# Optimization experiments

Measured on AMD Instinct MI355X. Metric: run time of the kernel, lower is better.

The kernel has to match this reference:

```python
import jax, jax.numpy as jnp
import numpy as np

N_NODES = 100000
N_EDGES = 1000000
N_GRAPHS = 512
HID = 64
EDIM = 32
LAYERS = 4
BN_EPS = 1e-5


def _batchnorm(x, g, b):
    # training-mode BatchNorm1d: biased batch statistics over the node axis
    m = x.mean(axis=0)
    v = jnp.var(x, axis=0)
    return (x - m) * jax.lax.rsqrt(v + BN_EPS) * g + b


def setup_inputs() -> dict:
    key = jax.random.key(0)
    ks = jax.random.split(key, 16)
    zw = 2 * HID + EDIM  # 160: cat([x_i, x_j, e_ij])
    inp = {
        "z": jax.random.randint(ks[0], (N_NODES,), 0, 100),
        "edge_index": jax.random.randint(ks[1], (2, N_EDGES), 0, N_NODES),
        "edge_attr": jax.random.normal(ks[2], (N_EDGES, EDIM), dtype=jnp.float32),
        "batch_ids": jnp.sort(jax.random.randint(ks[3], (N_NODES,), 0, N_GRAPHS)),
        "emb": jax.random.normal(ks[4], (100, HID), dtype=jnp.float32),
        "Wf": jax.random.normal(ks[5], (LAYERS, zw, HID), dtype=jnp.float32) / np.sqrt(zw),
        "bf": jnp.zeros((LAYERS, HID), jnp.float32),
        "Ws": jax.random.normal(ks[6], (LAYERS, zw, HID), dtype=jnp.float32) / np.sqrt(zw),
        "bs": jnp.zeros((LAYERS, HID), jnp.float32),
        "g_cbn": jnp.ones((LAYERS, HID), jnp.float32),
        "b_cbn": jnp.zeros((LAYERS, HID), jnp.float32),
        "g_obn": jnp.ones((LAYERS, HID), jnp.float32),
        "b_obn": jnp.zeros((LAYERS, HID), jnp.float32),
        "W1": jax.random.normal(ks[7], (HID, HID), dtype=jnp.float32) / np.sqrt(HID),
        "b1": jnp.zeros((HID,), jnp.float32),
        "W2": jax.random.normal(ks[8], (HID, 1), dtype=jnp.float32) / np.sqrt(HID),
        "b2": jnp.zeros((1,), jnp.float32),
    }
    return inp


def reference(z, edge_index, edge_attr, batch_ids, emb, Wf, bf, Ws, bs,
              g_cbn, b_cbn, g_obn, b_obn, W1, b1, W2, b2):
    src = edge_index[0]  # x_j (source)
    dst = edge_index[1]  # x_i (target / aggregation index)
    x = emb[z]  # [N, HID]
    for l in range(LAYERS):
        # CGConv message: z_e = cat([x_i, x_j, e_ij]); m = sigmoid(f(z_e)) * softplus(s(z_e))
        z_e = jnp.concatenate([x[dst], x[src], edge_attr], axis=-1)  # [E, 160]
        msg = jax.nn.sigmoid(z_e @ Wf[l] + bf[l]) * jax.nn.softplus(z_e @ Ws[l] + bs[l])
        agg = jax.ops.segment_sum(msg, dst, num_segments=N_NODES)  # [N, HID]
        agg = _batchnorm(agg, g_cbn[l], b_cbn[l])  # CGConv's internal BN
        x = agg + x  # residual
        x = _batchnorm(x, g_obn[l], b_obn[l])  # outer BatchNorm1d
        x = jax.nn.softplus(x)
    # global mean pool over graphs
    sums = jax.ops.segment_sum(x, batch_ids, num_segments=N_GRAPHS)
    cnts = jax.ops.segment_sum(jnp.ones((N_NODES,), x.dtype), batch_ids, num_segments=N_GRAPHS)
    pooled = sums / jnp.maximum(cnts, 1.0)[:, None]
    h = jax.nn.silu(pooled @ W1 + b1)  # dropout is identity in eval mode
    out = (h @ W2 + b2)[:, 0]
    return out
```

## Files before the change

### kernel.cpp

```cpp
#include <hip/hip_runtime.h>
#include <cstdint>
#include <cstddef>

#define N_NODES 100000
#define N_EDGES 1000000
#define N_GRAPHS 512
#define HID 64
#define EDIM 32
#define LAYERS 4
#define BN_EPS 1e-5
#define NPB 1024

static const size_t X_OFF    = 0;
static const size_t AGG_OFF  = 25600000;
static const size_t STA_OFF  = 51200000;
static const size_t STB_OFF  = 51201024;
static const size_t POOL_OFF = 51202048;
static const size_t CNT_OFF  = 51333120;
static const size_t DEG_OFF  = 51335168;
static const size_t ECUR_OFF = 51735296;
static const size_t PERM_OFF = 52135424;
static const size_t DSTS_OFF = 56135424;
static const size_t SRCS_OFF = 60135424;
static const size_t BSUM_OFF = 64135424;
static const size_t BOFF_OFF = 64137472;
static const size_t PART_OFF = 64139520;
static const size_t P_OFF    = 64663808;

#define SCAN_BLOCKS 391

__device__ __forceinline__ float rl_f(float v, int k) {
    return __uint_as_float(__builtin_amdgcn_readlane(__float_as_uint(v), k));
}
__device__ __forceinline__ float sigmoidf_(float x) {
    return 1.f / (1.f + __expf(-x));
}
__device__ __forceinline__ float softplusf_(float x) {
    return fmaxf(x, 0.f) + __logf(1.f + __expf(-fabsf(x)));
}
__device__ __forceinline__ void fma4(float4& a, const float4& wv, float xv) {
    a.x = fmaf(xv, wv.x, a.x);
    a.y = fmaf(xv, wv.y, a.y);
    a.z = fmaf(xv, wv.z, a.z);
    a.w = fmaf(xv, wv.w, a.w);
}

__global__ __launch_bounds__(256) void cg_embed(const int* __restrict__ z,
                                                const float* __restrict__ emb,
                                                float* __restrict__ x) {
    int i = blockIdx.x * 256 + threadIdx.x;
    if (i < N_NODES * HID) {
        x[i] = emb[z[i >> 6] * HID + (i & 63)];
    }
}

__global__ __launch_bounds__(256) void cg_hist(const int* __restrict__ ei,
                                               int* __restrict__ deg) {
    int e = blockIdx.x * 256 + threadIdx.x;
    if (e < N_EDGES) atomicAdd(&deg[ei[N_EDGES + e]], 1);
}

__global__ __launch_bounds__(256) void cg_bsum(const int* __restrict__ deg,
                                               int* __restrict__ bsum) {
    const int i = blockIdx.x * 256 + threadIdx.x;
    int v = (i < N_NODES) ? deg[i] : 0;
#pragma unroll
    for (int off = 32; off > 0; off >>= 1) v += __shfl_down(v, off);
    __shared__ int wsum[4];
    if ((threadIdx.x & 63) == 0) wsum[threadIdx.x >> 6] = v;
    __syncthreads();
    if (threadIdx.x == 0) bsum[blockIdx.x] = wsum[0] + wsum[1] + wsum[2] + wsum[3];
}

__global__ __launch_bounds__(512) void cg_bscan(const int* __restrict__ bsum,
                                                int* __restrict__ boff) {
    __shared__ int ps[512];
    const int t = threadIdx.x;
    int v = (t < SCAN_BLOCKS) ? bsum[t] : 0;
    ps[t] = v;
    __syncthreads();
    for (int off = 1; off < 512; off <<= 1) {
        int u = (t >= off) ? ps[t - off] : 0;
        __syncthreads();
        ps[t] += u;
        __syncthreads();
    }
    if (t < SCAN_BLOCKS) boff[t] = ps[t] - v;
}

__global__ __launch_bounds__(256) void cg_escan(const int* __restrict__ deg,
                                                const int* __restrict__ boff,
                                                int* __restrict__ ecur) {
    __shared__ int ps[256];
    const int t = threadIdx.x;
    const int i = blockIdx.x * 256 + t;
    int v = (i < N_NODES) ? deg[i] : 0;
    ps[t] = v;
    __syncthreads();
    for (int off = 1; off < 256; off <<= 1) {
        int u = (t >= off) ? ps[t - off] : 0;
        __syncthreads();
        ps[t] += u;
        __syncthreads();
    }
    if (i < N_NODES) ecur[i] = ps[t] - v + boff[blockIdx.x];
}

__global__ __launch_bounds__(256) void cg_scatter(const int* __restrict__ ei,
                                                  int* __restrict__ ecur,
                                                  int* __restrict__ perm,
                                                  int* __restrict__ dst_s,
                                                  int* __restrict__ src_s) {
    int e = blockIdx.x * 256 + threadIdx.x;
    if (e < N_EDGES) {
        int d = ei[N_EDGES + e];
        int pos = atomicAdd(&ecur[d], 1);
        perm[pos] = e;
        dst_s[pos] = d;
        src_s[pos] = ei[e];
    }
}

__global__ __launch_bounds__(256, 2) void cg_nodeP4(const float* __restrict__ x,
                                                    const float* __restrict__ Wf,
                                                    const float* __restrict__ Ws,
                                                    float* __restrict__ P) {
    __shared__ __align__(16) float xs[64][68];
    const int tid = threadIdx.x;
    const int base = blockIdx.x * 64;
#pragma unroll
    for (int i = 0; i < 4; i++) {
        int f4 = tid * 4 + i;
        int r = f4 >> 4, c4 = (f4 & 15) * 4;
        float4 v = {0, 0, 0, 0};
        if (base + r < N_NODES) v = *(const float4*)(x + (size_t)(base + r) * HID + c4);
        *(float4*)(&xs[r][c4]) = v;
    }
    __syncthreads();

    const int g = tid >> 4;
    const int j4 = (tid & 15) * 4;
    float4 acc[4][4];
#pragma unroll
    for (int m = 0; m < 4; m++)
#pragma unroll
        for (int q = 0; q < 4; q++) acc[m][q] = {0, 0, 0, 0};

    for (int k = 0; k < 64; k++) {
        float4 w0 = *(const float4*)(Wf + (size_t)k * HID + j4);
        float4 w1 = *(const float4*)(Ws + (size_t)k * HID + j4);
        float4 w2 = *(const float4*)(Wf + (size_t)(64 + k) * HID + j4);
        float4 w3 = *(const float4*)(Ws + (size_t)(64 + k) * HID + j4);
#pragma unroll
        for (int m = 0; m < 4; m++) {
            float xv = xs[g + m * 16][k];
            fma4(acc[m][0], w0, xv);
            fma4(acc[m][1], w1, xv);
            fma4(acc[m][2], w2, xv);
            fma4(acc[m][3], w3, xv);
        }
    }
#pragma unroll
    for (int m = 0; m < 4; m++) {
        int r = base + g + m * 16;
        if (r < N_NODES) {
            float* o = P + (size_t)r * 256;
            *(float4*)(o + j4)       = acc[m][0];
            *(float4*)(o + 64 + j4)  = acc[m][1];
            *(float4*)(o + 128 + j4) = acc[m][2];
            *(float4*)(o + 192 + j4) = acc[m][3];
        }
    }
}

__global__ __launch_bounds__(256, 4) void cg_edge4(const float* __restrict__ P,
                                                   const float* __restrict__ ea,
                                                   const int* __restrict__ perm,
                                                   const int* __restrict__ dst_s,
                                                   const int* __restrict__ src_s,
                                                   const float* __restrict__ WfE,
                                                   const float* __restrict__ WsE,
                                                   const float* __restrict__ bf,
                                                   const float* __restrict__ bs,
                                                   float* __restrict__ agg) {
    const int j = threadIdx.x & 63;
    float wfe[EDIM], wse[EDIM];
#pragma unroll
    for (int k = 0; k < EDIM; k++) wfe[k] = WfE[k * HID + j];
#pragma unroll
    for (int k = 0; k < EDIM; k++) wse[k] = WsE[k * HID + j];
#pragma unroll
    for (int k = 0; k < EDIM; k++) {
        asm volatile("" : "+v"(wfe[k]));
        asm volatile("" : "+v"(wse[k]));
    }
    const float bfv = bf[j], bsv = bs[j];

    const int wave = blockIdx.x * 4 + (threadIdx.x >> 6);
    const int nw = gridDim.x * 4;
    const int chunk = (N_EDGES + nw - 1) / nw;
    const int e0 = wave * chunk;
    const int e1 = min(e0 + chunk, N_EDGES);
    if (e0 >= e1) return;

    int eu = __builtin_amdgcn_readfirstlane(e0);
    int d_c  = dst_s[eu];
    int s_c  = src_s[eu];
    int pe_c = perm[eu];
    float sf_c = P[(size_t)s_c * 256 + 128 + j];
    float ss_c = P[(size_t)s_c * 256 + 192 + j];

    int cur = __builtin_amdgcn_readfirstlane(d_c);
    float pf0 = P[(size_t)cur * 256 + j];
    float ps0 = P[(size_t)cur * 256 + 64 + j];
    float acc = 0.f;

    for (int e = e0; e < e1; ++e) {
        const int d  = __builtin_amdgcn_readfirstlane(d_c);
        const int pe = __builtin_amdgcn_readfirstlane(pe_c);
        const float sf = sf_c, ss = ss_c;
        const float* __restrict__ er = ea + (size_t)pe * EDIM;
        float e_r[EDIM];
#pragma unroll
        for (int k = 0; k < EDIM; k++) e_r[k] = er[k];
        if (e + 1 < e1) {
            int nu = __builtin_amdgcn_readfirstlane(e + 1);
            d_c  = dst_s[nu];
            s_c  = src_s[nu];
            pe_c = perm[nu];
            sf_c = P[(size_t)s_c * 256 + 128 + j];
            ss_c = P[(size_t)s_c * 256 + 192 + j];
        }
        if (d != cur) {
            unsafeAtomicAdd(&agg[(size_t)cur * HID + j], acc);
            acc = 0.f;
            cur = d;
            pf0 = P[(size_t)cur * 256 + j];
            ps0 = P[(size_t)cur * 256 + 64 + j];
        }
        float uf0 = bfv + pf0, uf1 = sf;
        float us0 = bsv + ps0, us1 = ss;
#pragma unroll
        for (int k = 0; k < EDIM; k += 2) {
            uf0 = fmaf(e_r[k], wfe[k], uf0);
            us0 = fmaf(e_r[k], wse[k], us0);
            uf1 = fmaf(e_r[k + 1], wfe[k + 1], uf1);
            us1 = fmaf(e_r[k + 1], wse[k + 1], us1);
        }
        acc += sigmoidf_(uf0 + uf1) * softplusf_(us0 + us1);
    }
    unsafeAtomicAdd(&agg[(size_t)cur * HID + j], acc);
}

__global__ __launch_bounds__(256) void cg_stats(const float* __restrict__ a,
                                                float* __restrict__ parts) {
    const int j = threadIdx.x & 63, rl = threadIdx.x >> 6;
    float s = 0.f, q = 0.f;
    for (int n = blockIdx.x * 4 + rl; n < N_NODES; n += gridDim.x * 4) {
        float v = a[(size_t)n * HID + j];
        s += v;
        q += v * v;
    }
    __shared__ float ls[4][64], lq[4][64];
    ls[rl][j] = s;
    lq[rl][j] = q;
    __syncthreads();
    if (threadIdx.x < 64) {
        float S = ls[0][j] + ls[1][j] + ls[2][j] + ls[3][j];
        float Q = lq[0][j] + lq[1][j] + lq[2][j] + lq[3][j];
        parts[(size_t)blockIdx.x * 128 + j] = S;
        parts[(size_t)blockIdx.x * 128 + 64 + j] = Q;
    }
}

__global__ __launch_bounds__(256) void cg_fin(const float* __restrict__ parts,
                                              double* __restrict__ st) {
    const int c = threadIdx.x & 127;
    const int h = threadIdx.x >> 7;
    double s = 0.0;
    for (int i = h * (NPB / 2); i < (h + 1) * (NPB / 2); i++)
        s += (double)parts[(size_t)i * 128 + c];
    __shared__ double sh[128];
    if (h == 0) sh[c] = s;
    __syncthreads();
    if (h == 1) st[c] = sh[c] + s;
}

__global__ __launch_bounds__(256) void cg_bn1res(float* __restrict__ agg,
                                                 const float* __restrict__ x,
                                                 const float* __restrict__ g,
                                                 const float* __restrict__ b,
                                                 const double* __restrict__ stA,
                                                 float* __restrict__ parts) {
    const int j = threadIdx.x & 63, rl = threadIdx.x >> 6;
    const double mean = stA[j] * (1.0 / N_NODES);
    const double var  = stA[64 + j] * (1.0 / N_NODES) - mean * mean;
    const float sc = (float)((double)g[j] / sqrt(var + BN_EPS));
    const float sh = (float)((double)b[j] - mean * (double)sc);
    float s = 0.f, q = 0.f;
    for (int n = blockIdx.x * 4 + rl; n < N_NODES; n += gridDim.x * 4) {
        size_t idx = (size_t)n * HID + j;
        float v = fmaf(agg[idx], sc, sh) + x[idx];
        agg[idx] = v;
        s += v;
        q += v * v;
    }
    __shared__ float ls[4][64], lq[4][64];
    ls[rl][j] = s;
    lq[rl][j] = q;
    __syncthreads();
    if (threadIdx.x < 64) {
        float S = ls[0][j] + ls[1][j] + ls[2][j] + ls[3][j];
        float Q = lq[0][j] + lq[1][j] + lq[2][j] + lq[3][j];
        parts[(size_t)blockIdx.x * 128 + j] = S;
        parts[(size_t)blockIdx.x * 128 + 64 + j] = Q;
    }
}

__global__ __launch_bounds__(256) void cg_bn2act(float* __restrict__ agg,
                                                 float* __restrict__ x,
                                                 const float* __restrict__ g,
                                                 const float* __restrict__ b,
                                                 const double* __restrict__ stB) {
    const int j = threadIdx.x & 63, rl = threadIdx.x >> 6;
    const double mean = stB[j] * (1.0 / N_NODES);
    const double var  = stB[64 + j] * (1.0 / N_NODES) - mean * mean;
    const float sc = (float)((double)g[j] / sqrt(var + BN_EPS));
    const float sh = (float)((double)b[j] - mean * (double)sc);
    for (int n = blockIdx.x * 4 + rl; n < N_NODES; n += gridDim.x * 4) {
        size_t idx = (size_t)n * HID + j;
        x[idx] = softplusf_(fmaf(agg[idx], sc, sh));
        agg[idx] = 0.f;
    }
}

__global__ __launch_bounds__(256) void cg_pool(const float* __restrict__ x,
                                               const int* __restrict__ bid,
                                               float* __restrict__ pooled,
                                               float* __restrict__ cnt) {
    const int j = threadIdx.x & 63, rl = threadIdx.x >> 6;
    const int chunk = (N_NODES + gridDim.x - 1) / gridDim.x;
    const int s0 = blockIdx.x * chunk;
    const int e0 = min(s0 + chunk, N_NODES);
    float acc = 0.f, c = 0.f;
    int cur = -1;
    for (int n = s0 + rl; n < e0; n += 4) {
        int bg = bid[n];
        if (bg != cur) {
            if (cur >= 0) {
                unsafeAtomicAdd(&pooled[(size_t)cur * HID + j], acc);
                if (j == 0) unsafeAtomicAdd(&cnt[cur], c);
            }
            cur = bg;
            acc = 0.f;
            c = 0.f;
        }
        acc += x[(size_t)n * HID + j];
        c += 1.f;
    }
    if (cur >= 0) {
        unsafeAtomicAdd(&pooled[(size_t)cur * HID + j], acc);
        if (j == 0) unsafeAtomicAdd(&cnt[cur], c);
    }
}

__global__ __launch_bounds__(64) void cg_mlp(const float* __restrict__ pooled,
                                             const float* __restrict__ cnt,
                                             const float* __restrict__ W1,
                                             const float* __restrict__ b1,
                                             const float* __restrict__ W2,
                                             const float* __restrict__ b2,
                                             float* __restrict__ out) {
    const int g = blockIdx.x;
    const int j = threadIdx.x;
    const float c = fmaxf(cnt[g], 1.f);
    const float p = pooled[(size_t)g * HID + j] / c;
    float h = b1[j];
    for (int k = 0; k < HID; k++) {
        h = fmaf(rl_f(p, k), W1[k * HID + j], h);
    }
    const float hs = h * sigmoidf_(h);
    float v = hs * W2[j];
#pragma unroll
    for (int off = 32; off > 0; off >>= 1) v += __shfl_down(v, off);
    if (j == 0) out[g] = v + b2[0];
}

extern "C" void kernel_launch(void* const* d_in, const int* in_sizes, int n_in,
                              void* d_out, int out_size, void* d_ws, size_t ws_size,
                              hipStream_t stream) {
    const int*   z   = (const int*)d_in[0];
    const int*   ei  = (const int*)d_in[1];
    const float* ea  = (const float*)d_in[2];
    const int*   bid = (const int*)d_in[3];
    const float* emb = (const float*)d_in[4];
    const float* Wf  = (const float*)d_in[5];
    const float* bf  = (const float*)d_in[6];
    const float* Ws  = (const float*)d_in[7];
    const float* bs  = (const float*)d_in[8];
    const float* gc  = (const float*)d_in[9];
    const float* bc  = (const float*)d_in[10];
    const float* go  = (const float*)d_in[11];
    const float* bo  = (const float*)d_in[12];
    const float* W1  = (const float*)d_in[13];
    const float* b1  = (const float*)d_in[14];
    const float* W2  = (const float*)d_in[15];
    const float* b2  = (const float*)d_in[16];
    float* out = (float*)d_out;

    char* ws = (char*)d_ws;
    float*  x      = (float*)(ws + X_OFF);
    float*  agg    = (float*)(ws + AGG_OFF);
    double* stA    = (double*)(ws + STA_OFF);
    double* stB    = (double*)(ws + STB_OFF);
    float*  pooled = (float*)(ws + POOL_OFF);
    float*  cnt    = (float*)(ws + CNT_OFF);
    int*    deg    = (int*)(ws + DEG_OFF);
    int*    ecur   = (int*)(ws + ECUR_OFF);
    int*    perm   = (int*)(ws + PERM_OFF);
    int*    dst_s  = (int*)(ws + DSTS_OFF);
    int*    src_s  = (int*)(ws + SRCS_OFF);
    int*    bsum   = (int*)(ws + BSUM_OFF);
    int*    boff   = (int*)(ws + BOFF_OFF);
    float*  parts  = (float*)(ws + PART_OFF);
    float*  P      = (float*)(ws + P_OFF);

    (void)hipMemsetAsync(ws + AGG_OFF, 0, 25600000, stream);
    (void)hipMemsetAsync(ws + POOL_OFF, 0, 131072 + 2048, stream);
    (void)hipMemsetAsync(ws + DEG_OFF, 0, 400000, stream);

    cg_hist<<<(N_EDGES + 255) / 256, 256, 0, stream>>>(ei, deg);
    cg_bsum<<<SCAN_BLOCKS, 256, 0, stream>>>(deg, bsum);
    cg_bscan<<<1, 512, 0, stream>>>(bsum, boff);
    cg_escan<<<SCAN_BLOCKS, 256, 0, stream>>>(deg, boff, ecur);
    cg_scatter<<<(N_EDGES + 255) / 256, 256, 0, stream>>>(ei, ecur, perm, dst_s, src_s);

    cg_embed<<<(N_NODES * HID + 255) / 256, 256, 0, stream>>>(z, emb, x);

    for (int l = 0; l < LAYERS; l++) {
        const float* Wfl = Wf + (size_t)l * 160 * HID;
        const float* Wsl = Ws + (size_t)l * 160 * HID;
        cg_nodeP4<<<(N_NODES + 63) / 64, 256, 0, stream>>>(x, Wfl, Wsl, P);
        cg_edge4<<<1024, 256, 0, stream>>>(P, ea, perm, dst_s, src_s,
                                           Wfl + 128 * HID, Wsl + 128 * HID,
                                           bf + l * HID, bs + l * HID, agg);
        cg_stats<<<NPB, 256, 0, stream>>>(agg, parts);
        cg_fin<<<1, 256, 0, stream>>>(parts, stA);
        cg_bn1res<<<NPB, 256, 0, stream>>>(agg, x, gc + l * HID, bc + l * HID, stA, parts);
        cg_fin<<<1, 256, 0, stream>>>(parts, stB);
        cg_bn2act<<<NPB, 256, 0, stream>>>(agg, x, go + l * HID, bo + l * HID, stB);
    }

    cg_pool<<<1024, 256, 0, stream>>>(x, bid, pooled, cnt);
    cg_mlp<<<N_GRAPHS, 64, 0, stream>>>(pooled, cnt, W1, b1, W2, b2, out);
}
```

Measured before the change: 2.203 ms.

## Software-pipeline edge attribute and destination loads in edge kernel; halve stats grid

The edge kernel now prefetches the next edge's attribute row (double-buffered between two register arrays), its destination node projections and its source projections one iteration ahead. Before, it loaded the current edge's 32 attributes at the top of the iteration and reloaded destination rows only when the segment changed. The aim is to hide the latency of these gathers behind the FMA work, at the cost of higher register pressure and a destination load on every edge. Separately, the stats and BN1 kernels now launch 512 blocks instead of 1024, while the BN2 kernel keeps 1024.

```diff
diff --git a/kernel.cpp b/kernel.cpp
--- a/kernel.cpp
+++ b/kernel.cpp
@@ -9,7 +9,7 @@
 #define EDIM 32
 #define LAYERS 4
 #define BN_EPS 1e-5
-#define NPB 1024
+#define NPB 512
 
 static const size_t X_OFF    = 0;
 static const size_t AGG_OFF  = 25600000;
@@ -173,7 +173,7 @@
     }
 }
 
-__global__ __launch_bounds__(256, 4) void cg_edge4(const float* __restrict__ P,
+__global__ __launch_bounds__(256, 4) void cg_edge5(const float* __restrict__ P,
                                                    const float* __restrict__ ea,
                                                    const int* __restrict__ perm,
                                                    const int* __restrict__ dst_s,
@@ -203,51 +203,62 @@
     const int e1 = min(e0 + chunk, N_EDGES);
     if (e0 >= e1) return;
 
-    int eu = __builtin_amdgcn_readfirstlane(e0);
-    int d_c  = dst_s[eu];
-    int s_c  = src_s[eu];
-    int pe_c = perm[eu];
+    int   d_c  = __builtin_amdgcn_readfirstlane(dst_s[e0]);
+    int   s_c  = __builtin_amdgcn_readfirstlane(src_s[e0]);
+    int   pe0  = __builtin_amdgcn_readfirstlane(perm[e0]);
     float sf_c = P[(size_t)s_c * 256 + 128 + j];
     float ss_c = P[(size_t)s_c * 256 + 192 + j];
-
-    int cur = __builtin_amdgcn_readfirstlane(d_c);
-    float pf0 = P[(size_t)cur * 256 + j];
-    float ps0 = P[(size_t)cur * 256 + 64 + j];
+    float pf_c = P[(size_t)d_c * 256 + j];
+    float ps_c = P[(size_t)d_c * 256 + 64 + j];
+    float erA[EDIM], erB[EDIM];
+#pragma unroll
+    for (int k = 0; k < EDIM; k++) erA[k] = ea[(size_t)pe0 * EDIM + k];
+
+    int cur = d_c;
+    float pf0 = pf_c, ps0 = ps_c;
     float acc = 0.f;
 
-    for (int e = e0; e < e1; ++e) {
-        const int d  = __builtin_amdgcn_readfirstlane(d_c);
-        const int pe = __builtin_amdgcn_readfirstlane(pe_c);
-        const float sf = sf_c, ss = ss_c;
-        const float* __restrict__ er = ea + (size_t)pe * EDIM;
-        float e_r[EDIM];
-#pragma unroll
-        for (int k = 0; k < EDIM; k++) e_r[k] = er[k];
+    auto body = [&](const float (&erC)[EDIM], float (&erN)[EDIM], int e) {
+        int d_n = d_c, s_n = s_c;
+        float sf_n = sf_c, ss_n = ss_c, pf_n = pf_c, ps_n = ps_c;
         if (e + 1 < e1) {
-            int nu = __builtin_amdgcn_readfirstlane(e + 1);
-            d_c  = dst_s[nu];
-            s_c  = src_s[nu];
-            pe_c = perm[nu];
-            sf_c = P[(size_t)s_c * 256 + 128 + j];
-            ss_c = P[(size_t)s_c * 256 + 192 + j];
-        }
-        if (d != cur) {
+            d_n = __builtin_amdgcn_readfirstlane(dst_s[e + 1]);
+            s_n = __builtin_amdgcn_readfirstlane(src_s[e + 1]);
+            int pe_n = __builtin_amdgcn_readfirstlane(perm[e + 1]);
+            sf_n = P[(size_t)s_n * 256 + 128 + j];
+            ss_n = P[(size_t)s_n * 256 + 192 + j];
+            pf_n = P[(size_t)d_n * 256 + j];
+            ps_n = P[(size_t)d_n * 256 + 64 + j];
+#pragma unroll
+            for (int k = 0; k < EDIM; k++) erN[k] = ea[(size_t)pe_n * EDIM + k];
+        }
+        if (d_c != cur) {
             unsafeAtomicAdd(&agg[(size_t)cur * HID + j], acc);
             acc = 0.f;
-            cur = d;
-            pf0 = P[(size_t)cur * 256 + j];
-            ps0 = P[(size_t)cur * 256 + 64 + j];
-        }
-        float uf0 = bfv + pf0, uf1 = sf;
-        float us0 = bsv + ps0, us1 = ss;
+            cur = d_c;
+            pf0 = pf_c;
+            ps0 = ps_c;
+        }
+        float uf0 = bfv + pf0, uf1 = sf_c;
+        float us0 = bsv + ps0, us1 = ss_c;
 #pragma unroll
         for (int k = 0; k < EDIM; k += 2) {
-            uf0 = fmaf(e_r[k], wfe[k], uf0);
-            us0 = fmaf(e_r[k], wse[k], us0);
-            uf1 = fmaf(e_r[k + 1], wfe[k + 1], uf1);
-            us1 = fmaf(e_r[k + 1], wse[k + 1], us1);
+            uf0 = fmaf(erC[k], wfe[k], uf0);
+            us0 = fmaf(erC[k], wse[k], us0);
+            uf1 = fmaf(erC[k + 1], wfe[k + 1], uf1);
+            us1 = fmaf(erC[k + 1], wse[k + 1], us1);
         }
         acc += sigmoidf_(uf0 + uf1) * softplusf_(us0 + us1);
+        d_c = d_n; s_c = s_n;
+        sf_c = sf_n; ss_c = ss_n; pf_c = pf_n; ps_c = ps_n;
+    };
+
+    for (int e = e0; e < e1;) {
+        body(erA, erB, e);
+        ++e;
+        if (e >= e1) break;
+        body(erB, erA, e);
+        ++e;
     }
     unsafeAtomicAdd(&agg[(size_t)cur * HID + j], acc);
 }
@@ -441,14 +452,14 @@
         const float* Wfl = Wf + (size_t)l * 160 * HID;
         const float* Wsl = Ws + (size_t)l * 160 * HID;
         cg_nodeP4<<<(N_NODES + 63) / 64, 256, 0, stream>>>(x, Wfl, Wsl, P);
-        cg_edge4<<<1024, 256, 0, stream>>>(P, ea, perm, dst_s, src_s,
+        cg_edge5<<<1024, 256, 0, stream>>>(P, ea, perm, dst_s, src_s,
                                            Wfl + 128 * HID, Wsl + 128 * HID,
                                            bf + l * HID, bs + l * HID, agg);
         cg_stats<<<NPB, 256, 0, stream>>>(agg, parts);
         cg_fin<<<1, 256, 0, stream>>>(parts, stA);
         cg_bn1res<<<NPB, 256, 0, stream>>>(agg, x, gc + l * HID, bc + l * HID, stA, parts);
         cg_fin<<<1, 256, 0, stream>>>(parts, stB);
-        cg_bn2act<<<NPB, 256, 0, stream>>>(agg, x, go + l * HID, bo + l * HID, stB);
+        cg_bn2act<<<1024, 256, 0, stream>>>(agg, x, go + l * HID, bo + l * HID, stB);
     }
 
     cg_pool<<<1024, 256, 0, stream>>>(x, bid, pooled, cnt);
```

New measurement: 7.581 ms. 244% more time.
